# Kernel tuning notes

Measured on AMD Instinct MI355X. Metric: run time of the kernel, lower is better.

Reference implementation:

```python
import jax, jax.numpy as jnp
import numpy as np

D_MODEL = 768
D_INNER = 1536      # expand=2
D_STATE = 16
DT_RANK = 48        # ceil(768/16)
D_CONV = 4
DEPTH = 24
NUM_CLASSES = 527
GRID = (8, 64)      # (128/16, 1024/16)
SEQ = GRID[0] * GRID[1]
TOKPOS = SEQ // 2   # middle cls token position


def setup_inputs() -> dict:
    key = jax.random.key(0)
    ks = jax.random.split(key, 12)
    rn = lambda k, s, sc=0.02: jax.random.normal(k, s, jnp.float32) * sc
    A_init = jnp.log(jnp.arange(1, D_STATE + 1, dtype=jnp.float32))  # S4D-real init
    return {
        "x": jax.random.normal(ks[0], (1, 1, 128, 1024), jnp.float32),
        "patch_w": rn(ks[1], (D_MODEL, 1, 16, 16)),
        "patch_b": jnp.zeros((D_MODEL,), jnp.float32),
        "cls_token": rn(ks[2], (1, 1, D_MODEL)),
        "pos_embed": rn(ks[3], (1, SEQ + 1, D_MODEL)),
        "in_proj_w": rn(ks[4], (DEPTH, 2 * D_INNER, D_MODEL)),
        "conv_w": rn(ks[5], (DEPTH, 2, D_INNER, D_CONV), 0.1),
        "conv_b": jnp.zeros((DEPTH, 2, D_INNER), jnp.float32),
        "xproj_w": rn(ks[6], (DEPTH, 2, DT_RANK + 2 * D_STATE, D_INNER)),
        "dtproj_w": rn(ks[7], (DEPTH, 2, D_INNER, DT_RANK), 0.1),
        "dtproj_b": jnp.full((DEPTH, 2, D_INNER), float(np.log(np.expm1(0.01))), jnp.float32),
        "A_log": jnp.ones((DEPTH, 2, D_INNER, 1), jnp.float32) * A_init,
        "D_skip": jnp.ones((DEPTH, 2, D_INNER), jnp.float32),
        "out_proj_w": rn(ks[8], (DEPTH, D_MODEL, D_INNER)),
        "norm_w": jnp.ones((DEPTH, D_MODEL), jnp.float32),
        "norm_f_w": jnp.ones((D_MODEL,), jnp.float32),
        "head_w": rn(ks[9], (NUM_CLASSES, D_MODEL)),
        "head_b": jnp.zeros((NUM_CLASSES,), jnp.float32),
    }


def _rmsnorm(x, w, eps=1e-5):
    return x * jax.lax.rsqrt(jnp.mean(x * x, axis=-1, keepdims=True) + eps) * w


def _causal_conv_silu(x, w, b):
    # x [B,d,L], depthwise causal conv, kernel D_CONV, left-pad D_CONV-1
    L = x.shape[-1]
    xp = jnp.pad(x, ((0, 0), (0, 0), (D_CONV - 1, 0)))
    y = sum(w[:, k, None] * xp[:, :, k:k + L] for k in range(D_CONV)) + b[:, None]
    return jax.nn.silu(y)


def _selective_scan(dt, A, Bm, C, u):
    # dt,u: [B,d,L]; Bm,C: [B,N,L]; A: [d,N] (negative)
    def step(h, inp):
        dt_t, B_t, C_t, u_t = inp           # [B,d],[B,N],[B,N],[B,d]
        h = h * jnp.exp(dt_t[..., None] * A) + (dt_t * u_t)[..., None] * B_t[:, None, :]
        return h, jnp.einsum('bdn,bn->bd', h, C_t)
    h0 = jnp.zeros((dt.shape[0], A.shape[0], A.shape[1]), dt.dtype)
    mv = lambda a: jnp.moveaxis(a, -1, 0)
    _, ys = jax.lax.scan(step, h0, (mv(dt), mv(Bm), mv(C), mv(u)))
    return jnp.moveaxis(ys, 0, -1)          # [B,d,L]


def _mamba_dir(x, z, cw, cb, xw, dw, db, A_log, Dsk):
    xc = _causal_conv_silu(x, cw, cb)
    dbl = jnp.einsum('bdl,cd->bcl', xc, xw)                 # [B, R+2N, L]
    dt = jax.nn.softplus(jnp.einsum('brl,dr->bdl', dbl[:, :DT_RANK], dw) + db[:, None])
    Bm = dbl[:, DT_RANK:DT_RANK + D_STATE]
    C = dbl[:, DT_RANK + D_STATE:]
    y = _selective_scan(dt, -jnp.exp(A_log), Bm, C, xc) + Dsk[:, None] * xc
    return y * jax.nn.silu(z)


def _block(carry, p):
    hidden, residual = carry
    ipw, cw, cb, xw, dw, db, A_log, Dsk, opw, nw = p
    residual = residual + hidden                            # add -> norm -> mixer
    h = _rmsnorm(residual, nw)
    xz = jnp.einsum('bld,ed->ble', h, ipw)                  # [B,L,2*d_inner]
    x, z = jnp.split(jnp.moveaxis(xz, -1, 1), 2, axis=1)    # each [B,d_inner,L]
    yf = _mamba_dir(x, z, cw[0], cb[0], xw[0], dw[0], db[0], A_log[0], Dsk[0])
    yb = _mamba_dir(x[:, :, ::-1], z[:, :, ::-1], cw[1], cb[1], xw[1], dw[1],
                    db[1], A_log[1], Dsk[1])[:, :, ::-1]
    out = jnp.einsum('bdl,ed->ble', (yf + yb) * 0.5, opw)   # if_devide_out
    return (out, residual), None


def reference(x, patch_w, patch_b, cls_token, pos_embed, in_proj_w, conv_w, conv_b,
              xproj_w, dtproj_w, dtproj_b, A_log, D_skip, out_proj_w, norm_w,
              norm_f_w, head_w, head_b):
    h = jax.lax.conv_general_dilated(x, patch_w, (16, 16), 'VALID',
                                     dimension_numbers=('NCHW', 'OIHW', 'NCHW'))
    h = h + patch_b[None, :, None, None]
    B = h.shape[0]
    h = h.reshape(B, D_MODEL, SEQ).transpose(0, 2, 1)       # [B,512,768]
    cls = jnp.broadcast_to(cls_token, (B, 1, D_MODEL))
    h = jnp.concatenate([h[:, :TOKPOS], cls, h[:, TOKPOS:]], axis=1)  # [B,513,768]
    h = h + pos_embed
    carry = (h, jnp.zeros_like(h))
    (hidden, residual), _ = jax.lax.scan(
        _block, carry,
        (in_proj_w, conv_w, conv_b, xproj_w, dtproj_w, dtproj_b, A_log, D_skip,
         out_proj_w, norm_w))
    out = _rmsnorm(residual + hidden, norm_f_w)
    feat = out[:, TOKPOS]                                   # middle cls token
    return feat @ head_w.T + head_b
```

## Files before the change

kernel.cpp:

```cpp
#include <hip/hip_runtime.h>

#define L_SEQ 513
#define DM 768
#define DI 1536
#define DSTATE 16
#define DTRANK 48
#define NCLS 527
#define DEPTH 24
#define NC 32
#define CLEN 17
#define SKI 3
#define SKO 8

typedef unsigned short u16;
typedef __bf16 bf16x8 __attribute__((ext_vector_type(8)));
typedef float f32x4 __attribute__((ext_vector_type(4)));

#define MFMA_BF16(A, B, C) __builtin_amdgcn_mfma_f32_16x16x32_bf16(A, B, C, 0, 0, 0)

__device__ inline u16 f2bf(float x) {
  unsigned u = __float_as_uint(x);
  return (u16)((u + 0x7FFFu + ((u >> 16) & 1u)) >> 16);
}
__device__ inline float bf2f(u16 h) { return __uint_as_float((unsigned)h << 16); }
__device__ inline void split2(float v, u16& h, u16& l) {
  h = f2bf(v);
  l = f2bf(v - bf2f(h));
}
__device__ __forceinline__ int lofs(int row, int g) {
  int swz = (row & 3) ^ ((row >> 2) & 3);
  return row * 32 + ((g ^ swz) << 3);
}

__global__ void wconvert_kernel(const float* __restrict__ src,
                                u16* __restrict__ hi, u16* __restrict__ lo,
                                long n4) {
  long i = (long)blockIdx.x * 256 + threadIdx.x;
  long stride = (long)gridDim.x * 256;
  for (; i < n4; i += stride) {
    float4 v = ((const float4*)src)[i];
    ushort4 h, l;
    split2(v.x, h.x, l.x);
    split2(v.y, h.y, l.y);
    split2(v.z, h.z, l.z);
    split2(v.w, h.w, l.w);
    ((ushort4*)hi)[i] = h;
    ((ushort4*)lo)[i] = l;
  }
}

__global__ void patch_embed_kernel(const float* __restrict__ x,
                                   const float* __restrict__ pw,
                                   const float* __restrict__ pb,
                                   const float* __restrict__ cls,
                                   const float* __restrict__ pos,
                                   float* __restrict__ hidden,
                                   float* __restrict__ residual) {
  int c = blockIdx.x * 256 + threadIdx.x;
  int s = blockIdx.y;
  if (c >= DM) return;
  float val;
  if (s == 256) {
    val = cls[c];
  } else {
    int p = s - (s > 256 ? 1 : 0);
    int gy = p >> 6, gx = p & 63;
    const float* xp = x + gy * 16 * 1024 + gx * 16;
    const float* wp = pw + c * 256;
    float acc = pb[c];
#pragma unroll 4
    for (int ky = 0; ky < 16; ++ky)
#pragma unroll
      for (int kx = 0; kx < 16; ++kx)
        acc += xp[ky * 1024 + kx] * wp[ky * 16 + kx];
    val = acc;
  }
  long idx = (long)s * DM + c;
  hidden[idx] = val + pos[idx];
  residual[idx] = 0.f;
}

__global__ void rmsnorm_kernel(const float* __restrict__ hp, int nparts, long pstr,
                               float* __restrict__ residual,
                               u16* __restrict__ hnh, u16* __restrict__ hnl,
                               const float* __restrict__ w) {
  int t = blockIdx.x;
  float* rrow = residual + (long)t * DM;
  int tid = threadIdx.x;
  float vals[3];
  float ss = 0.f;
#pragma unroll
  for (int i = 0; i < 3; ++i) {
    int c = tid + i * 256;
    float v = rrow[c];
    for (int p = 0; p < nparts; ++p) v += hp[(long)p * pstr + (long)t * DM + c];
    vals[i] = v;
    rrow[c] = v;
    ss += v * v;
  }
#pragma unroll
  for (int o = 32; o; o >>= 1) ss += __shfl_down(ss, o, 64);
  __shared__ float sacc[4];
  if ((tid & 63) == 0) sacc[tid >> 6] = ss;
  __syncthreads();
  float tot = sacc[0] + sacc[1] + sacc[2] + sacc[3];
  float rs = rsqrtf(tot / (float)DM + 1e-5f);
#pragma unroll
  for (int i = 0; i < 3; ++i) {
    int c = tid + i * 256;
    float y = vals[i] * rs * w[c];
    u16 h, l;
    split2(y, h, l);
    hnh[(long)t * DM + c] = h;
    hnl[(long)t * DM + c] = l;
  }
}

template <int AMODE>
__global__ __launch_bounds__(256) void gemm128(
    const void* __restrict__ A0, const void* __restrict__ A1,
    const u16* __restrict__ Bh, const u16* __restrict__ Bl,
    float* __restrict__ C,
    int M, int N, int K, int lda, int ldb, int ldc,
    long sA, long sB, long sC, int NSK, int Kb, long sP) {
  int z = blockIdx.z;
  int batch = z / NSK, sk = z - batch * NSK;
  const u16* Ahb = nullptr;
  const u16* Alb = nullptr;
  const float* Af = nullptr;
  const float* Ag = nullptr;
  if (AMODE == 0) {
    Ahb = (const u16*)A0 + (long)batch * sA;
    Alb = (const u16*)A1 + (long)batch * sA;
  } else {
    Af = (const float*)A0 + (long)batch * sA;
    Ag = (const float*)A1 + (long)batch * sA;
  }
  const u16* Bhb = Bh + (long)batch * sB;
  const u16* Blb = Bl + (long)batch * sB;
  float* Cb = C + (long)batch * sC + (long)sk * sP;
  int ks0 = sk * Kb;
  int kend = min(ks0 + Kb, K);

  __shared__ u16 SA[2][2][128 * 32];
  __shared__ u16 SB[2][2][128 * 32];

  int tid = threadIdx.x;
  int m0 = blockIdx.y * 128, n0 = blockIdx.x * 128;

  int r0 = tid >> 2, g0 = tid & 3;
  int r1 = r0 + 64;
  int l0 = lofs(r0, g0), l1 = lofs(r1, g0);
  long aoff0 = (long)(m0 + r0) * lda, aoff1 = (long)(m0 + r1) * lda;
  long boff0 = (long)(n0 + r0) * ldb, boff1 = (long)(n0 + r1) * ldb;
  bool am0 = (m0 + r0) < M, am1 = (m0 + r1) < M;
  bool bm0 = (n0 + r0) < N, bm1 = (n0 + r1) < N;

  int lane = tid & 63, w = tid >> 6;
  int wr = w >> 1, wc = w & 1;
  int fr = lane & 15, kh = lane >> 4;
  int offA[4], offB[4];
#pragma unroll
  for (int i = 0; i < 4; ++i) {
    offA[i] = lofs(wr * 64 + i * 16 + fr, kh);
    offB[i] = lofs(wc * 64 + i * 16 + fr, kh);
  }

// ... 22 lines not shown
      ll = *(const uint4*)la;
    }
  };
  auto loadstep = [&](int kb) {
    int k_ = kb + g0 * 8;
    bool kk = (k_ + 8 <= kend);
    uint4 z4 = {0, 0, 0, 0};
    loadA(aoff0, kk && am0, k_, a0h, a0l);
    loadA(aoff1, kk && am1, k_, a1h, a1l);
    b0h = (kk && bm0) ? *(const uint4*)(Bhb + boff0 + k_) : z4;
    b1h = (kk && bm1) ? *(const uint4*)(Bhb + boff1 + k_) : z4;
    b0l = (kk && bm0) ? *(const uint4*)(Blb + boff0 + k_) : z4;
    b1l = (kk && bm1) ? *(const uint4*)(Blb + boff1 + k_) : z4;
  };
  auto writebuf = [&](int b) {
    *(uint4*)&SA[b][0][l0] = a0h;
    *(uint4*)&SA[b][0][l1] = a1h;
    *(uint4*)&SA[b][1][l0] = a0l;
    *(uint4*)&SA[b][1][l1] = a1l;
    *(uint4*)&SB[b][0][l0] = b0h;
    *(uint4*)&SB[b][0][l1] = b1h;
    *(uint4*)&SB[b][1][l0] = b0l;
    *(uint4*)&SB[b][1][l1] = b1l;
  };

  f32x4 acc[4][4] = {};
  int nst = (kend - ks0 + 31) >> 5;
  loadstep(ks0);
  writebuf(0);
  if (nst > 1) loadstep(ks0 + 32);
  __syncthreads();

  for (int s = 0; s < nst; ++s) {
    int b = s & 1;
    bf16x8 fah[4], fal[4], fbh[4], fbl[4];
#pragma unroll
    for (int i = 0; i < 4; ++i) {
      fah[i] = __builtin_bit_cast(bf16x8, *(const uint4*)&SA[b][0][offA[i]]);
      fal[i] = __builtin_bit_cast(bf16x8, *(const uint4*)&SA[b][1][offA[i]]);
      fbh[i] = __builtin_bit_cast(bf16x8, *(const uint4*)&SB[b][0][offB[i]]);
      fbl[i] = __builtin_bit_cast(bf16x8, *(const uint4*)&SB[b][1][offB[i]]);
    }
#pragma unroll
    for (int mi = 0; mi < 4; ++mi)
#pragma unroll
      for (int ni = 0; ni < 4; ++ni) {
        acc[mi][ni] = MFMA_BF16(fah[mi], fbh[ni], acc[mi][ni]);
        acc[mi][ni] = MFMA_BF16(fah[mi], fbl[ni], acc[mi][ni]);
        acc[mi][ni] = MFMA_BF16(fal[mi], fbh[ni], acc[mi][ni]);
      }
    if (s + 1 < nst) {
      writebuf(b ^ 1);
      if (s + 2 < nst) loadstep(ks0 + (s + 2) * 32);
    }
    __syncthreads();
  }

#pragma unroll
  for (int mi = 0; mi < 4; ++mi)
#pragma unroll
    for (int ni = 0; ni < 4; ++ni) {
      int n = n0 + wc * 64 + ni * 16 + fr;
      if (n >= N) continue;
#pragma unroll
      for (int r = 0; r < 4; ++r) {
        int m = m0 + wr * 64 + mi * 16 + kh * 4 + r;
        if (m >= M) continue;
        Cb[(long)m * ldc + n] = acc[mi][ni][r];
      }
    }
}

__global__ void conv_silu_kernel(const float* __restrict__ xz_p,
                                 const float* __restrict__ cw,
                                 const float* __restrict__ cb,
                                 float* __restrict__ xc,
                                 u16* __restrict__ xch, u16* __restrict__ xcl) {
  const long PZ = (long)L_SEQ * 2 * DI;
  int dir = blockIdx.y;
  int idx = blockIdx.x * 256 + threadIdx.x;
  if (idx >= L_SEQ * (DI / 4)) return;
  int d4 = idx % (DI / 4);
  int t = idx / (DI / 4);
  int d = d4 * 4;
  float wv[4][4];
#pragma unroll
  for (int j = 0; j < 4; ++j) {
    float4 wr = *(const float4*)(cw + ((long)dir * DI + d + j) * 4);
    wv[j][0] = wr.x; wv[j][1] = wr.y; wv[j][2] = wr.z; wv[j][3] = wr.w;
  }
  float4 bv = *(const float4*)(cb + (long)dir * DI + d);
  float a0 = bv.x, a1 = bv.y, a2 = bv.z, a3 = bv.w;
#pragma unroll
  for (int k = 0; k < 4; ++k) {
    int tau = t + k - 3;
    if (tau >= 0) {
      int tsrc = dir ? (L_SEQ - 1 - tau) : tau;
      long o = (long)tsrc * (2 * DI) + d;
      float4 x0 = *(const float4*)(xz_p + o);
      float4 x1 = *(const float4*)(xz_p + o + PZ);
      float4 x2 = *(const float4*)(xz_p + o + 2 * PZ);
      a0 += wv[0][k] * (x0.x + x1.x + x2.x);
      a1 += wv[1][k] * (x0.y + x1.y + x2.y);
      a2 += wv[2][k] * (x0.z + x1.z + x2.z);
      a3 += wv[3][k] * (x0.w + x1.w + x2.w);
    }
  }
  float4 sv;
  sv.x = a0 / (1.f + __expf(-a0));
  sv.y = a1 / (1.f + __expf(-a1));
  sv.z = a2 / (1.f + __expf(-a2));
  sv.w = a3 / (1.f + __expf(-a3));
  long o = ((long)dir * L_SEQ + t) * DI + d;
  *(float4*)(xc + o) = sv;
  ushort4 h, l;
  split2(sv.x, h.x, l.x);
  split2(sv.y, h.y, l.y);
  split2(sv.z, h.z, l.z);
  split2(sv.w, h.w, l.w);
  *(ushort4*)(xch + o) = h;
  *(ushort4*)(xcl + o) = l;
}

__global__ __launch_bounds__(256) void scan_all(
    const float* __restrict__ xc,
    const float* __restrict__ dbl,
    const float* __restrict__ xz_p,
    const float* __restrict__ dtw,
    const float* __restrict__ dtb,
    const float* __restrict__ A_log,
    const float* __restrict__ Dsk,
    float* __restrict__ y) {
  const long PZ = (long)L_SEQ * 2 * DI;
  int dir = blockIdx.y;
  int d0 = blockIdx.x * 8;
  int tid = threadIdx.x;
  __shared__ float Q[8][NC][DSTATE];
  __shared__ float Sv[8][NC];

  const float* xcp = xc + (long)dir * L_SEQ * DI;
  const float* dblp = dbl + (long)dir * L_SEQ * 80;

  int dl = tid & 7, c = tid >> 3;
  int d = d0 + dl;
  float negA[DSTATE];
#pragma unroll
  for (int n = 0; n < DSTATE; ++n)
    negA[n] = -__expf(A_log[((long)dir * DI + d) * DSTATE + n]);
  float4 dwr[12];
  {
    const float4* dwp = (const float4*)(dtw + ((long)dir * DI + d) * DTRANK);
#pragma unroll
    for (int q = 0; q < 12; ++q) dwr[q] = dwp[q];
  }
  float db_ = dtb[(long)dir * DI + d];

  int t0 = c * CLEN, t1 = min(t0 + CLEN, L_SEQ);

  {
    float h[DSTATE];
#pragma unroll
    for (int n = 0; n < DSTATE; ++n) h[n] = 0.f;
    float S = 0.f;
    for (int t = t0; t < t1; ++t) {
      const float4* R = (const float4*)(dblp + (long)t * 80);
      float dot = db_;
#pragma unroll
      for (int q = 0; q < 12; ++q) {
        float4 r4 = R[q];
        dot += r4.x * dwr[q].x + r4.y * dwr[q].y + r4.z * dwr[q].z + r4.w * dwr[q].w;
      }
      float dt = (dot > 20.f) ? dot : log1pf(__expf(dot));
      float u = xcp[(long)t * DI + d];
      float du = dt * u;
      S += dt;
      float4 b0 = R[12], b1 = R[13], b2 = R[14], b3 = R[15];
      float Bv[DSTATE] = {b0.x, b0.y, b0.z, b0.w, b1.x, b1.y, b1.z, b1.w,
                          b2.x, b2.y, b2.z, b2.w, b3.x, b3.y, b3.z, b3.w};
#pragma unroll
      for (int n = 0; n < DSTATE; ++n)
        h[n] = h[n] * __expf(dt * negA[n]) + du * Bv[n];
    }
    Sv[dl][c] = S;
#pragma unroll
    for (int n = 0; n < DSTATE; ++n) Q[dl][c][n] = h[n];
  }
  __syncthreads();
  if (tid < 128) {
    int fdl = tid >> 4, n = tid & 15;
    int fd = d0 + fdl;
    float nA = -__expf(A_log[((long)dir * DI + fd) * DSTATE + n]);
    float h = 0.f;
    for (int cc = 0; cc < NC; ++cc) {
      float S = Sv[fdl][cc];
      float q = Q[fdl][cc][n];
      Q[fdl][cc][n] = h;
      h = h * __expf(nA * S) + q;
    }
  }
  __syncthreads();
  {
    float h[DSTATE];
#pragma unroll
    for (int n = 0; n < DSTATE; ++n) h[n] = Q[dl][c][n];
    float dskip = Dsk[(long)dir * DI + d];
    for (int t = t0; t < t1; ++t) {
      const float4* R = (const float4*)(dblp + (long)t * 80);
      float dot = db_;
#pragma unroll
      for (int q = 0; q < 12; ++q) {
        float4 r4 = R[q];
        dot += r4.x * dwr[q].x + r4.y * dwr[q].y + r4.z * dwr[q].z + r4.w * dwr[q].w;
      }
      float dt = (dot > 20.f) ? dot : log1pf(__expf(dot));
      float u = xcp[(long)t * DI + d];
      float du = dt * u;
      float4 b0 = R[12], b1 = R[13], b2 = R[14], b3 = R[15];
      float4 c0 = R[16], c1 = R[17], c2 = R[18], c3 = R[19];
      float Bv[DSTATE] = {b0.x, b0.y, b0.z, b0.w, b1.x, b1.y, b1.z, b1.w,
                          b2.x, b2.y, b2.z, b2.w, b3.x, b3.y, b3.z, b3.w};
      float Cv[DSTATE] = {c0.x, c0.y, c0.z, c0.w, c1.x, c1.y, c1.z, c1.w,
                          c2.x, c2.y, c2.z, c2.w, c3.x, c3.y, c3.z, c3.w};
      float acc = 0.f;
#pragma unroll
      for (int n = 0; n < DSTATE; ++n) {
        h[n] = h[n] * __expf(dt * negA[n]) + du * Bv[n];
        acc += h[n] * Cv[n];
      }
      int tsrc = dir ? (L_SEQ - 1 - t) : t;
      long zo = (long)tsrc * (2 * DI) + DI + d;
      float zv = xz_p[zo] + xz_p[zo + PZ] + xz_p[zo + 2 * PZ];
      float sz = zv / (1.f + __expf(-zv));
      y[((long)dir * L_SEQ + tsrc) * DI + d] = (acc + dskip * u) * sz;
    }
  }
}

__global__ void head_kernel(const float* __restrict__ residual,
                            const float* __restrict__ hp, long pstr,
                            const float* __restrict__ nfw,
                            const float* __restrict__ hw,
                            const float* __restrict__ hb,
                            float* __restrict__ out) {
  int j = blockIdx.x;
  int tid = threadIdx.x;
  const float* r = residual + (long)256 * DM;
  float ss = 0.f, dp = 0.f;
#pragma unroll
  for (int i = 0; i < 3; ++i) {
    int c = tid + i * 256;
    float v = r[c];
    for (int p = 0; p < SKO; ++p) v += hp[(long)p * pstr + (long)256 * DM + c];
    ss += v * v;
    dp += v * nfw[c] * hw[(long)j * DM + c];
  }
#pragma unroll
  for (int o = 32; o; o >>= 1) {
    ss += __shfl_down(ss, o, 64);
    dp += __shfl_down(dp, o, 64);
  }
  __shared__ float s1[4], s2[4];
  if ((tid & 63) == 0) {
    s1[tid >> 6] = ss;
    s2[tid >> 6] = dp;
  }
  __syncthreads();
  if (tid == 0) {
    float tot = s1[0] + s1[1] + s1[2] + s1[3];
    float d = s2[0] + s2[1] + s2[2] + s2[3];
    out[j] = d * rsqrtf(tot / (float)DM + 1e-5f) + hb[j];
  }
}

extern "C" void kernel_launch(void* const* d_in, const int* in_sizes, int n_in,
                              void* d_out, int out_size, void* d_ws, size_t ws_size,
                              hipStream_t stream) {
  const float* x        = (const float*)d_in[0];
  const float* patch_w  = (const float*)d_in[1];
  const float* patch_b  = (const float*)d_in[2];
  const float* cls_tok  = (const float*)d_in[3];
  const float* pos_emb  = (const float*)d_in[4];
  const float* in_proj  = (const float*)d_in[5];
  const float* conv_w   = (const float*)d_in[6];
  const float* conv_b   = (const float*)d_in[7];
  const float* xproj_w  = (const float*)d_in[8];
  const float* dtproj_w = (const float*)d_in[9];
  const float* dtproj_b = (const float*)d_in[10];
  const float* A_log    = (const float*)d_in[11];
  const float* D_skip   = (const float*)d_in[12];
  const float* out_proj = (const float*)d_in[13];
  const float* norm_w   = (const float*)d_in[14];
  const float* norm_f_w = (const float*)d_in[15];
  const float* head_w   = (const float*)d_in[16];
  const float* head_b   = (const float*)d_in[17];
  float* out = (float*)d_out;

  const long PHN = (long)L_SEQ * DM;
  const long PZ  = (long)L_SEQ * 2 * DI;

  float* ws = (float*)d_ws;
  float* residual = ws; ws += PHN;
  float* xz_p     = ws; ws += SKI * PZ;
  float* xc       = ws; ws += (long)2 * L_SEQ * DI;
  float* dbl      = ws; ws += (long)2 * L_SEQ * 80;
  float* yb       = ws; ws += (long)2 * L_SEQ * DI;
  float* hid_p    = ws; ws += (long)SKO * PHN;

  u16* wsu = (u16*)ws;
  const long N_HN = PHN;
  const long N_XC = (long)2 * L_SEQ * DI;
  const long N_WI = (long)DEPTH * 2 * DI * DM;
  const long N_WX = (long)DEPTH * 2 * 80 * DI;
  const long N_WO = (long)DEPTH * DM * DI;
  u16* hn_h = wsu; wsu += N_HN;
  u16* hn_l = wsu; wsu += N_HN;
  u16* xc_h = wsu; wsu += N_XC;
  u16* xc_l = wsu; wsu += N_XC;
  u16* wi_h = wsu; wsu += N_WI;
  u16* wi_l = wsu; wsu += N_WI;
  u16* wx_h = wsu; wsu += N_WX;
  u16* wx_l = wsu; wsu += N_WX;
  u16* wo_h = wsu; wsu += N_WO;
  u16* wo_l = wsu; wsu += N_WO;

  wconvert_kernel<<<2048, 256, 0, stream>>>(in_proj,  wi_h, wi_l, N_WI / 4);
  wconvert_kernel<<<512,  256, 0, stream>>>(xproj_w,  wx_h, wx_l, N_WX / 4);
  wconvert_kernel<<<2048, 256, 0, stream>>>(out_proj, wo_h, wo_l, N_WO / 4);

  patch_embed_kernel<<<dim3(3, L_SEQ), 256, 0, stream>>>(
      x, patch_w, patch_b, cls_tok, pos_emb, hid_p, residual);

  for (int l = 0; l < DEPTH; ++l) {
    const u16* wih = wi_h + (long)l * 2 * DI * DM;
    const u16* wil = wi_l + (long)l * 2 * DI * DM;
    const u16* wxh = wx_h + (long)l * 2 * 80 * DI;
    const u16* wxl = wx_l + (long)l * 2 * 80 * DI;
    const u16* woh = wo_h + (long)l * DM * DI;
    const u16* wol = wo_l + (long)l * DM * DI;
    const float* cw  = conv_w   + (long)l * 2 * DI * 4;
    const float* cb  = conv_b   + (long)l * 2 * DI;
    const float* dw  = dtproj_w + (long)l * 2 * DI * DTRANK;
    const float* db  = dtproj_b + (long)l * 2 * DI;
    const float* Al  = A_log    + (long)l * 2 * DI * DSTATE;
    const float* Dk  = D_skip   + (long)l * 2 * DI;
    const float* nw  = norm_w   + (long)l * DM;

    rmsnorm_kernel<<<L_SEQ, 256, 0, stream>>>(
        hid_p, (l == 0) ? 1 : SKO, PHN, residual, hn_h, hn_l, nw);

    gemm128<0><<<dim3(24, 5, SKI), 256, 0, stream>>>(
        hn_h, hn_l, wih, wil, xz_p, L_SEQ, 2 * DI, DM, DM, DM, 2 * DI,
        0, 0, 0, SKI, DM / SKI, PZ);

    conv_silu_kernel<<<dim3(770, 2), 256, 0, stream>>>(xz_p, cw, cb, xc, xc_h, xc_l);

    gemm128<0><<<dim3(1, 5, 2), 256, 0, stream>>>(
        xc_h, xc_l, wxh, wxl, dbl, L_SEQ, 80, DI, DI, DI, 80,
        (long)L_SEQ * DI, (long)80 * DI, (long)L_SEQ * 80, 1, DI, 0);

    scan_all<<<dim3(DI / 8, 2), 256, 0, stream>>>(
        xc, dbl, xz_p, dw, db, Al, Dk, yb);

    gemm128<1><<<dim3(6, 5, SKO), 256, 0, stream>>>(
        yb, yb + (long)L_SEQ * DI, woh, wol, hid_p, L_SEQ, DM, DI, DI, DI, DM,
        0, 0, 0, SKO, DI / SKO, PHN);
  }

  head_kernel<<<NCLS, 256, 0, stream>>>(residual, hid_p, PHN,
                                        norm_f_w, head_w, head_b, out);
}
```

Before: 4.750 ms.

## Fuse all layers into a persistent megakernel with software grid barriers

Replaces the per-layer sequence of six kernel launches with one persistent kernel of 256 blocks that loops over all 24 layers. Stages are separated by an atomic-flag grid barrier, which removes roughly 144 launch gaps. The dt projection becomes an MFMA GEMM with a fused softplus epilogue, z-gating SiLU is precomputed in the conv stage, and the in_proj split-K drops from 3 to 2. The cost is low parallelism in small stages such as the 10-tile x_proj GEMM and the scan, which leave most blocks idle. The software barrier also depends on all 256 blocks being co-resident.

```diff
diff --git a/kernel.cpp b/kernel.cpp
--- a/kernel.cpp
+++ b/kernel.cpp
@@ -9,10 +9,12 @@
 #define DEPTH 24
 #define NC 32
 #define CLEN 17
-#define SKI 3
+#define SKI 2
 #define SKO 8
+#define NBLK 256
 
 typedef unsigned short u16;
+typedef unsigned int u32;
 typedef __bf16 bf16x8 __attribute__((ext_vector_type(8)));
 typedef float f32x4 __attribute__((ext_vector_type(4)));
 
@@ -31,126 +33,51 @@
   int swz = (row & 3) ^ ((row >> 2) & 3);
   return row * 32 + ((g ^ swz) << 3);
 }
-
-__global__ void wconvert_kernel(const float* __restrict__ src,
-                                u16* __restrict__ hi, u16* __restrict__ lo,
-                                long n4) {
-  long i = (long)blockIdx.x * 256 + threadIdx.x;
-  long stride = (long)gridDim.x * 256;
-  for (; i < n4; i += stride) {
-    float4 v = ((const float4*)src)[i];
-    ushort4 h, l;
-    split2(v.x, h.x, l.x);
-    split2(v.y, h.y, l.y);
-    split2(v.z, h.z, l.z);
-    split2(v.w, h.w, l.w);
-    ((ushort4*)hi)[i] = h;
-    ((ushort4*)lo)[i] = l;
+__device__ inline float siluf(float v) { return v / (1.f + __expf(-v)); }
+
+__device__ __forceinline__ void grid_sync(u32* flags, u32* epoch, u32 e) {
+  __syncthreads();
+  if (blockIdx.x == 0) {
+    if (threadIdx.x == 0)
+      __hip_atomic_store(&flags[0], e, __ATOMIC_RELEASE, __HIP_MEMORY_SCOPE_AGENT);
+    int b = threadIdx.x;
+    while (__hip_atomic_load(&flags[b * 16], __ATOMIC_ACQUIRE, __HIP_MEMORY_SCOPE_AGENT) < e)
+      __builtin_amdgcn_s_sleep(1);
+    __syncthreads();
+    if (threadIdx.x == 0)
+      __hip_atomic_store(epoch, e, __ATOMIC_RELEASE, __HIP_MEMORY_SCOPE_AGENT);
+  } else {
+    if (threadIdx.x == 0) {
+      __hip_atomic_store(&flags[blockIdx.x * 16], e, __ATOMIC_RELEASE, __HIP_MEMORY_SCOPE_AGENT);
+      while (__hip_atomic_load(epoch, __ATOMIC_ACQUIRE, __HIP_MEMORY_SCOPE_AGENT) < e)
+        __builtin_amdgcn_s_sleep(1);
+    }
   }
-}
-
-__global__ void patch_embed_kernel(const float* __restrict__ x,
-                                   const float* __restrict__ pw,
-                                   const float* __restrict__ pb,
-                                   const float* __restrict__ cls,
-                                   const float* __restrict__ pos,
-                                   float* __restrict__ hidden,
-                                   float* __restrict__ residual) {
-  int c = blockIdx.x * 256 + threadIdx.x;
-  int s = blockIdx.y;
-  if (c >= DM) return;
-  float val;
-  if (s == 256) {
-    val = cls[c];
-  } else {
-    int p = s - (s > 256 ? 1 : 0);
-    int gy = p >> 6, gx = p & 63;
-    const float* xp = x + gy * 16 * 1024 + gx * 16;
-    const float* wp = pw + c * 256;
-    float acc = pb[c];
-#pragma unroll 4
-    for (int ky = 0; ky < 16; ++ky)
-#pragma unroll
-      for (int kx = 0; kx < 16; ++kx)
-        acc += xp[ky * 1024 + kx] * wp[ky * 16 + kx];
-    val = acc;
-  }
-  long idx = (long)s * DM + c;
-  hidden[idx] = val + pos[idx];
-  residual[idx] = 0.f;
-}
-
-__global__ void rmsnorm_kernel(const float* __restrict__ hp, int nparts, long pstr,
-                               float* __restrict__ residual,
-                               u16* __restrict__ hnh, u16* __restrict__ hnl,
-                               const float* __restrict__ w) {
-  int t = blockIdx.x;
-  float* rrow = residual + (long)t * DM;
+  __syncthreads();
+}
+
+template <int AMODE>
+__device__ void gemm_tile(const void* A0, const void* A1,
+                          const u16* __restrict__ Bh, const u16* __restrict__ Bl,
+                          float* __restrict__ Cb, int M, int N, int K,
+                          int lda, int ldb, int ldc,
+                          int m0, int n0, int ks0, int kend,
+                          const float* biasp, int act,
+                          u16* d48h, u16* d48l, int ncap, int ldhl,
+                          u16* LDSU) {
+  u16* SA = LDSU;
+  u16* SB = LDSU + 16384;
+
   int tid = threadIdx.x;
-  float vals[3];
-  float ss = 0.f;
-#pragma unroll
-  for (int i = 0; i < 3; ++i) {
-    int c = tid + i * 256;
-    float v = rrow[c];
-    for (int p = 0; p < nparts; ++p) v += hp[(long)p * pstr + (long)t * DM + c];
-    vals[i] = v;
-    rrow[c] = v;
-    ss += v * v;
-  }
-#pragma unroll
-  for (int o = 32; o; o >>= 1) ss += __shfl_down(ss, o, 64);
-  __shared__ float sacc[4];
-  if ((tid & 63) == 0) sacc[tid >> 6] = ss;
-  __syncthreads();
-  float tot = sacc[0] + sacc[1] + sacc[2] + sacc[3];
-  float rs = rsqrtf(tot / (float)DM + 1e-5f);
-#pragma unroll
-  for (int i = 0; i < 3; ++i) {
-    int c = tid + i * 256;
-    float y = vals[i] * rs * w[c];
-    u16 h, l;
-    split2(y, h, l);
-    hnh[(long)t * DM + c] = h;
-    hnl[(long)t * DM + c] = l;
-  }
-}
-
-template <int AMODE>
-__global__ __launch_bounds__(256) void gemm128(
-    const void* __restrict__ A0, const void* __restrict__ A1,
-    const u16* __restrict__ Bh, const u16* __restrict__ Bl,
-    float* __restrict__ C,
-    int M, int N, int K, int lda, int ldb, int ldc,
-    long sA, long sB, long sC, int NSK, int Kb, long sP) {
-  int z = blockIdx.z;
-  int batch = z / NSK, sk = z - batch * NSK;
-  const u16* Ahb = nullptr;
-  const u16* Alb = nullptr;
-  const float* Af = nullptr;
-  const float* Ag = nullptr;
-  if (AMODE == 0) {
-    Ahb = (const u16*)A0 + (long)batch * sA;
-    Alb = (const u16*)A1 + (long)batch * sA;
-  } else {
-    Af = (const float*)A0 + (long)batch * sA;
-    Ag = (const float*)A1 + (long)batch * sA;
-  }
-  const u16* Bhb = Bh + (long)batch * sB;
-  const u16* Blb = Bl + (long)batch * sB;
-  float* Cb = C + (long)batch * sC + (long)sk * sP;
-  int ks0 = sk * Kb;
-  int kend = min(ks0 + Kb, K);
-
-  __shared__ u16 SA[2][2][128 * 32];
-  __shared__ u16 SB[2][2][128 * 32];
-
-  int tid = threadIdx.x;
-  int m0 = blockIdx.y * 128, n0 = blockIdx.x * 128;
-
   int r0 = tid >> 2, g0 = tid & 3;
   int r1 = r0 + 64;
   int l0 = lofs(r0, g0), l1 = lofs(r1, g0);
+  const u16* Ahb = (const u16*)A0;
+  const u16* Alb = (const u16*)A1;
+  const float* Af = (const float*)A0;
+  const float* Ag = (const float*)A1;
+  const u16* Bhb = Bh;
+  const u16* Blb = Bl;
   long aoff0 = (long)(m0 + r0) * lda, aoff1 = (long)(m0 + r1) * lda;
   long boff0 = (long)(n0 + r0) * ldb, boff1 = (long)(n0 + r1) * ldb;
   bool am0 = (m0 + r0) < M, am1 = (m0 + r1) < M;
@@ -203,14 +130,14 @@
     b1l = (kk && bm1) ? *(const uint4*)(Blb + boff1 + k_) : z4;
   };
   auto writebuf = [&](int b) {
-    *(uint4*)&SA[b][0][l0] = a0h;
-    *(uint4*)&SA[b][0][l1] = a1h;
-    *(uint4*)&SA[b][1][l0] = a0l;
-    *(uint4*)&SA[b][1][l1] = a1l;
-    *(uint4*)&SB[b][0][l0] = b0h;
-    *(uint4*)&SB[b][0][l1] = b1h;
-    *(uint4*)&SB[b][1][l0] = b0l;
-    *(uint4*)&SB[b][1][l1] = b1l;
+    *(uint4*)&SA[((b << 1) | 0) * 4096 + l0] = a0h;
+    *(uint4*)&SA[((b << 1) | 0) * 4096 + l1] = a1h;
+    *(uint4*)&SA[((b << 1) | 1) * 4096 + l0] = a0l;
+    *(uint4*)&SA[((b << 1) | 1) * 4096 + l1] = a1l;
+    *(uint4*)&SB[((b << 1) | 0) * 4096 + l0] = b0h;
+    *(uint4*)&SB[((b << 1) | 0) * 4096 + l1] = b1h;
+    *(uint4*)&SB[((b << 1) | 1) * 4096 + l0] = b0l;
+    *(uint4*)&SB[((b << 1) | 1) * 4096 + l1] = b1l;
   };
 
   f32x4 acc[4][4] = {};
@@ -225,10 +152,10 @@
     bf16x8 fah[4], fal[4], fbh[4], fbl[4];
 #pragma unroll
     for (int i = 0; i < 4; ++i) {
-      fah[i] = __builtin_bit_cast(bf16x8, *(const uint4*)&SA[b][0][offA[i]]);
-      fal[i] = __builtin_bit_cast(bf16x8, *(const uint4*)&SA[b][1][offA[i]]);
-      fbh[i] = __builtin_bit_cast(bf16x8, *(const uint4*)&SB[b][0][offB[i]]);
-      fbl[i] = __builtin_bit_cast(bf16x8, *(const uint4*)&SB[b][1][offB[i]]);
+      fah[i] = __builtin_bit_cast(bf16x8, *(const uint4*)&SA[((b << 1) | 0) * 4096 + offA[i]]);
+      fal[i] = __builtin_bit_cast(bf16x8, *(const uint4*)&SA[((b << 1) | 1) * 4096 + offA[i]]);
+      fbh[i] = __builtin_bit_cast(bf16x8, *(const uint4*)&SB[((b << 1) | 0) * 4096 + offB[i]]);
+      fbl[i] = __builtin_bit_cast(bf16x8, *(const uint4*)&SB[((b << 1) | 1) * 4096 + offB[i]]);
     }
 #pragma unroll
     for (int mi = 0; mi < 4; ++mi)
@@ -251,213 +178,360 @@
     for (int ni = 0; ni < 4; ++ni) {
       int n = n0 + wc * 64 + ni * 16 + fr;
       if (n >= N) continue;
+      float bv = biasp ? biasp[n] : 0.f;
 #pragma unroll
       for (int r = 0; r < 4; ++r) {
         int m = m0 + wr * 64 + mi * 16 + kh * 4 + r;
         if (m >= M) continue;
-        Cb[(long)m * ldc + n] = acc[mi][ni][r];
-      }
-    }
-}
-
-__global__ void conv_silu_kernel(const float* __restrict__ xz_p,
-                                 const float* __restrict__ cw,
-                                 const float* __restrict__ cb,
-                                 float* __restrict__ xc,
-                                 u16* __restrict__ xch, u16* __restrict__ xcl) {
+        float v = acc[mi][ni][r] + bv;
+        if (act == 1) v = (v > 20.f) ? v : log1pf(__expf(v));
+        Cb[(long)m * ldc + n] = v;
+        if (d48h && n < ncap) {
+          u16 hh, ll;
+          split2(v, hh, ll);
+          d48h[(long)m * ldhl + n] = hh;
+          d48l[(long)m * ldhl + n] = ll;
+        }
+      }
+    }
+}
+
+__global__ void wconvert_kernel(const float* __restrict__ src,
+                                u16* __restrict__ hi, u16* __restrict__ lo,
+                                long n4) {
+  long i = (long)blockIdx.x * 256 + threadIdx.x;
+  long stride = (long)gridDim.x * 256;
+  for (; i < n4; i += stride) {
+    float4 v = ((const float4*)src)[i];
+    ushort4 h, l;
+    split2(v.x, h.x, l.x);
+    split2(v.y, h.y, l.y);
+    split2(v.z, h.z, l.z);
+    split2(v.w, h.w, l.w);
+    ((ushort4*)hi)[i] = h;
+    ((ushort4*)lo)[i] = l;
+  }
+}
+
+__global__ void patch_embed_kernel(const float* __restrict__ x,
+                                   const float* __restrict__ pw,
+                                   const float* __restrict__ pb,
+                                   const float* __restrict__ cls,
+                                   const float* __restrict__ pos,
+                                   float* __restrict__ hidden,
+                                   float* __restrict__ residual) {
+  int c = blockIdx.x * 256 + threadIdx.x;
+  int s = blockIdx.y;
+  if (c >= DM) return;
+  float val;
+  if (s == 256) {
+    val = cls[c];
+  } else {
+    int p = s - (s > 256 ? 1 : 0);
+    int gy = p >> 6, gx = p & 63;
+    const float* xp = x + gy * 16 * 1024 + gx * 16;
+    const float* wp = pw + c * 256;
+    float acc = pb[c];
+#pragma unroll 4
+    for (int ky = 0; ky < 16; ++ky)
+#pragma unroll
+      for (int kx = 0; kx < 16; ++kx)
+        acc += xp[ky * 1024 + kx] * wp[ky * 16 + kx];
+    val = acc;
+  }
+  long idx = (long)s * DM + c;
+  hidden[idx] = val + pos[idx];
+  residual[idx] = 0.f;
+}
+
+__global__ __launch_bounds__(256, 2) void mega(
+    const float* __restrict__ conv_w, const float* __restrict__ conv_b,
+    const float* __restrict__ dtproj_b, const float* __restrict__ A_log,
+    const float* __restrict__ D_skip, const float* __restrict__ norm_w,
+    const float* __restrict__ norm_f_w, const float* __restrict__ head_w,
+    const float* __restrict__ head_b,
+    float* residual, float* xz_p, float* xc, float* zs, float* dbl,
+    float* dtb, float* yb, float* hid_p,
+    u16* hn_h, u16* hn_l, u16* xc_h, u16* xc_l, u16* d48_h, u16* d48_l,
+    const u16* wi_h, const u16* wi_l, const u16* wx_h, const u16* wx_l,
+    const u16* wd_h, const u16* wd_l, const u16* wo_h, const u16* wo_l,
+    u32* flags, u32* epoch, float* out) {
+  __shared__ __align__(16) u16 LDSU[32768];
+  const int bid = blockIdx.x;
+  const int tid = threadIdx.x;
+  const long PHN = (long)L_SEQ * DM;
   const long PZ = (long)L_SEQ * 2 * DI;
-  int dir = blockIdx.y;
-  int idx = blockIdx.x * 256 + threadIdx.x;
-  if (idx >= L_SEQ * (DI / 4)) return;
-  int d4 = idx % (DI / 4);
-  int t = idx / (DI / 4);
-  int d = d4 * 4;
-  float wv[4][4];
-#pragma unroll
-  for (int j = 0; j < 4; ++j) {
-    float4 wr = *(const float4*)(cw + ((long)dir * DI + d + j) * 4);
-    wv[j][0] = wr.x; wv[j][1] = wr.y; wv[j][2] = wr.z; wv[j][3] = wr.w;
+  const long LDIlen = (long)L_SEQ * DI;
+  u32 e = 0;
+
+  for (int l = 0; l < DEPTH; ++l) {
+    const u16* wih = wi_h + (long)l * 2 * DI * DM;
+    const u16* wil = wi_l + (long)l * 2 * DI * DM;
+    const u16* wxh = wx_h + (long)l * 2 * 80 * DI;
+    const u16* wxl = wx_l + (long)l * 2 * 80 * DI;
+    const u16* wdh = wd_h + (long)l * 2 * DI * DTRANK;
+    const u16* wdl = wd_l + (long)l * 2 * DI * DTRANK;
+    const u16* woh = wo_h + (long)l * DM * DI;
+    const u16* wol = wo_l + (long)l * DM * DI;
+    const float* cw = conv_w + (long)l * 2 * DI * 4;
+    const float* cb = conv_b + (long)l * 2 * DI;
+    const float* db = dtproj_b + (long)l * 2 * DI;
+    const float* Al = A_log + (long)l * 2 * DI * DSTATE;
+    const float* Dk = D_skip + (long)l * 2 * DI;
+    const float* nw = norm_w + (long)l * DM;
+    int nparts = (l == 0) ? 1 : SKO;
+
+    for (int t = bid; t < L_SEQ; t += NBLK) {
+      float* rrow = residual + (long)t * DM;
+      float vals[3];
+      float ss = 0.f;
+#pragma unroll
+      for (int i = 0; i < 3; ++i) {
+        int c = tid + i * 256;
+        float v = rrow[c];
+        for (int p = 0; p < nparts; ++p) v += hid_p[(long)p * PHN + (long)t * DM + c];
+        vals[i] = v;
+        rrow[c] = v;
+        ss += v * v;
+      }
+#pragma unroll
+      for (int o = 32; o; o >>= 1) ss += __shfl_down(ss, o, 64);
+      float* sacc = (float*)LDSU;
+      if ((tid & 63) == 0) sacc[tid >> 6] = ss;
+      __syncthreads();
+      float tot = sacc[0] + sacc[1] + sacc[2] + sacc[3];
+      float rs = rsqrtf(tot / (float)DM + 1e-5f);
+      __syncthreads();
+#pragma unroll
+      for (int i = 0; i < 3; ++i) {
+        int c = tid + i * 256;
+        float y = vals[i] * rs * nw[c];
+        u16 h, lo;
+        split2(y, h, lo);
+        hn_h[(long)t * DM + c] = h;
+        hn_l[(long)t * DM + c] = lo;
+      }
+    }
+    e++; grid_sync(flags, epoch, e);
+
+    for (int vt = bid; vt < 24 * 5 * SKI; vt += NBLK) {
+      int sk = vt & (SKI - 1), rest = vt >> 1;
+      int my = rest / 24, nx = rest % 24;
+      gemm_tile<0>(hn_h, hn_l, wih, wil, xz_p + (long)sk * PZ,
+                   L_SEQ, 2 * DI, DM, DM, DM, 2 * DI,
+                   my * 128, nx * 128, sk * 384, min(DM, sk * 384 + 384),
+                   nullptr, 0, nullptr, nullptr, 0, 0, LDSU);
+    }
+    e++; grid_sync(flags, epoch, e);
+
+    for (int v = bid; v < 2310; v += NBLK) {
+      if (v < 1540) {
+        int dir = v / 770, vv = v - dir * 770;
+        int idx = vv * 256 + tid;
+        if (idx < L_SEQ * (DI / 4)) {
+          int d4 = idx % (DI / 4);
+          int t = idx / (DI / 4);
+          int d = d4 * 4;
+          float wv[4][4];
+#pragma unroll
+          for (int j = 0; j < 4; ++j) {
+            float4 wr4 = *(const float4*)(cw + ((long)dir * DI + d + j) * 4);
+            wv[j][0] = wr4.x; wv[j][1] = wr4.y; wv[j][2] = wr4.z; wv[j][3] = wr4.w;
+          }
+          float4 bv = *(const float4*)(cb + (long)dir * DI + d);
+          float a0 = bv.x, a1 = bv.y, a2 = bv.z, a3 = bv.w;
+#pragma unroll
+          for (int k = 0; k < 4; ++k) {
+            int tau = t + k - 3;
+            if (tau >= 0) {
+              int tsrc = dir ? (L_SEQ - 1 - tau) : tau;
+              long o = (long)tsrc * (2 * DI) + d;
+              float4 x0 = *(const float4*)(xz_p + o);
+              float4 x1 = *(const float4*)(xz_p + o + PZ);
+              a0 += wv[0][k] * (x0.x + x1.x);
+              a1 += wv[1][k] * (x0.y + x1.y);
+              a2 += wv[2][k] * (x0.z + x1.z);
+              a3 += wv[3][k] * (x0.w + x1.w);
+            }
+          }
+          float4 sv;
+          sv.x = siluf(a0); sv.y = siluf(a1); sv.z = siluf(a2); sv.w = siluf(a3);
+          long o = ((long)dir * L_SEQ + t) * DI + d;
+          *(float4*)(xc + o) = sv;
+          ushort4 h, lo;
+          split2(sv.x, h.x, lo.x);
+          split2(sv.y, h.y, lo.y);
+          split2(sv.z, h.z, lo.z);
+          split2(sv.w, h.w, lo.w);
+          *(ushort4*)(xc_h + o) = h;
+          *(ushort4*)(xc_l + o) = lo;
+        }
+      } else {
+        int vv = v - 1540;
+        int idx = vv * 256 + tid;
+        if (idx < L_SEQ * (DI / 4)) {
+          int d4 = idx % (DI / 4);
+          int t = idx / (DI / 4);
+          long zo = (long)t * (2 * DI) + DI + d4 * 4;
+          float4 z0 = *(const float4*)(xz_p + zo);
+          float4 z1 = *(const float4*)(xz_p + zo + PZ);
+          float4 sv;
+          sv.x = siluf(z0.x + z1.x);
+          sv.y = siluf(z0.y + z1.y);
+          sv.z = siluf(z0.z + z1.z);
+          sv.w = siluf(z0.w + z1.w);
+          *(float4*)(zs + (long)t * DI + d4 * 4) = sv;
+        }
+      }
+    }
+    e++; grid_sync(flags, epoch, e);
+
+    if (bid < 10) {
+      int dir = bid / 5, my = bid % 5;
+      gemm_tile<0>(xc_h + dir * LDIlen, xc_l + dir * LDIlen,
+                   wxh + (long)dir * 80 * DI, wxl + (long)dir * 80 * DI,
+                   dbl + (long)dir * L_SEQ * 80,
+                   L_SEQ, 80, DI, DI, DI, 80,
+                   my * 128, 0, 0, DI,
+                   nullptr, 0,
+                   d48_h + (long)dir * L_SEQ * DTRANK,
+                   d48_l + (long)dir * L_SEQ * DTRANK, DTRANK, DTRANK, LDSU);
+    }
+    e++; grid_sync(flags, epoch, e);
+
+    for (int vt = bid; vt < 120; vt += NBLK) {
+      int dir = vt / 60, r = vt - dir * 60;
+      int my = r / 12, nx = r % 12;
+      gemm_tile<0>(d48_h + (long)dir * L_SEQ * DTRANK, d48_l + (long)dir * L_SEQ * DTRANK,
+                   wdh + (long)dir * DI * DTRANK, wdl + (long)dir * DI * DTRANK,
+                   dtb + dir * LDIlen,
+                   L_SEQ, DI, DTRANK, DTRANK, DTRANK, DI,
+                   my * 128, nx * 128, 0, DTRANK,
+                   db + dir * DI, 1, nullptr, nullptr, 0, 0, LDSU);
+    }
+    e++; grid_sync(flags, epoch, e);
+
+    for (int vb = bid; vb < 384; vb += NBLK) {
+      int dir = vb / 192, d0 = (vb - dir * 192) * 8;
+      float* Q = (float*)LDSU;
+      float* Sv = (float*)LDSU + 4096;
+      const float* dtp = dtb + dir * LDIlen;
+      const float* xcp = xc + dir * LDIlen;
+      const float* dblp = dbl + (long)dir * L_SEQ * 80;
+      int dl = tid & 7, c = tid >> 3;
+      int d = d0 + dl;
+      float negA[DSTATE];
+#pragma unroll
+      for (int n = 0; n < DSTATE; ++n)
+        negA[n] = -__expf(Al[((long)dir * DI + d) * DSTATE + n]);
+      int t0 = c * CLEN, t1 = min(t0 + CLEN, L_SEQ);
+      {
+        float h[DSTATE];
+#pragma unroll
+        for (int n = 0; n < DSTATE; ++n) h[n] = 0.f;
+        float S = 0.f;
+        for (int t = t0; t < t1; ++t) {
+          float dt = dtp[(long)t * DI + d];
+          float u = xcp[(long)t * DI + d];
+          float du = dt * u;
+          S += dt;
+          const float4* B4 = (const float4*)(dblp + (long)t * 80 + DTRANK);
+          float4 b0 = B4[0], b1 = B4[1], b2 = B4[2], b3 = B4[3];
+          float Bv[DSTATE] = {b0.x, b0.y, b0.z, b0.w, b1.x, b1.y, b1.z, b1.w,
+                              b2.x, b2.y, b2.z, b2.w, b3.x, b3.y, b3.z, b3.w};
+#pragma unroll
+          for (int n = 0; n < DSTATE; ++n)
+            h[n] = h[n] * __expf(dt * negA[n]) + du * Bv[n];
+        }
+        Sv[dl * NC + c] = S;
+#pragma unroll
+        for (int n = 0; n < DSTATE; ++n) Q[(dl * NC + c) * DSTATE + n] = h[n];
+      }
+      __syncthreads();
+      if (tid < 128) {
+        int fdl = tid >> 4, n = tid & 15;
+        int fd = d0 + fdl;
+        float nA = -__expf(Al[((long)dir * DI + fd) * DSTATE + n]);
+        float h = 0.f;
+        for (int cc = 0; cc < NC; ++cc) {
+          float S = Sv[fdl * NC + cc];
+          float q = Q[(fdl * NC + cc) * DSTATE + n];
+          Q[(fdl * NC + cc) * DSTATE + n] = h;
+          h = h * __expf(nA * S) + q;
+        }
+      }
+      __syncthreads();
+      {
+        float h[DSTATE];
+#pragma unroll
+        for (int n = 0; n < DSTATE; ++n) h[n] = Q[(dl * NC + c) * DSTATE + n];
+        float dskip = Dk[(long)dir * DI + d];
+        for (int t = t0; t < t1; ++t) {
+          float dt = dtp[(long)t * DI + d];
+          float u = xcp[(long)t * DI + d];
+          float du = dt * u;
+          const float4* B4 = (const float4*)(dblp + (long)t * 80 + DTRANK);
+          float4 b0 = B4[0], b1 = B4[1], b2 = B4[2], b3 = B4[3];
+          float4 c0 = B4[4], c1 = B4[5], c2 = B4[6], c3 = B4[7];
+          float Bv[DSTATE] = {b0.x, b0.y, b0.z, b0.w, b1.x, b1.y, b1.z, b1.w,
+                              b2.x, b2.y, b2.z, b2.w, b3.x, b3.y, b3.z, b3.w};
+          float Cv[DSTATE] = {c0.x, c0.y, c0.z, c0.w, c1.x, c1.y, c1.z, c1.w,
+                              c2.x, c2.y, c2.z, c2.w, c3.x, c3.y, c3.z, c3.w};
+          float acc = 0.f;
+#pragma unroll
+          for (int n = 0; n < DSTATE; ++n) {
+            h[n] = h[n] * __expf(dt * negA[n]) + du * Bv[n];
+            acc += h[n] * Cv[n];
+          }
+          int tsrc = dir ? (L_SEQ - 1 - t) : t;
+          float sz = zs[(long)tsrc * DI + d];
+          yb[((long)dir * L_SEQ + tsrc) * DI + d] = (acc + dskip * u) * sz;
+        }
+      }
+      __syncthreads();
+    }
+    e++; grid_sync(flags, epoch, e);
+
+    for (int vt = bid; vt < 240; vt += NBLK) {
+      int sk = vt & 7, rest = vt >> 3;
+      int my = rest / 6, nx = rest % 6;
+      gemm_tile<1>(yb, yb + LDIlen, woh, wol, hid_p + (long)sk * PHN,
+                   L_SEQ, DM, DI, DI, DI, DM,
+                   my * 128, nx * 128, sk * 192, sk * 192 + 192,
+                   nullptr, 0, nullptr, nullptr, 0, 0, LDSU);
+    }
+    e++; grid_sync(flags, epoch, e);
   }
-  float4 bv = *(const float4*)(cb + (long)dir * DI + d);
-  float a0 = bv.x, a1 = bv.y, a2 = bv.z, a3 = bv.w;
-#pragma unroll
-  for (int k = 0; k < 4; ++k) {
-    int tau = t + k - 3;
-    if (tau >= 0) {
-      int tsrc = dir ? (L_SEQ - 1 - tau) : tau;
-      long o = (long)tsrc * (2 * DI) + d;
-      float4 x0 = *(const float4*)(xz_p + o);
-      float4 x1 = *(const float4*)(xz_p + o + PZ);
-      float4 x2 = *(const float4*)(xz_p + o + 2 * PZ);
-      a0 += wv[0][k] * (x0.x + x1.x + x2.x);
-      a1 += wv[1][k] * (x0.y + x1.y + x2.y);
-      a2 += wv[2][k] * (x0.z + x1.z + x2.z);
-      a3 += wv[3][k] * (x0.w + x1.w + x2.w);
-    }
-  }
-  float4 sv;
-  sv.x = a0 / (1.f + __expf(-a0));
-  sv.y = a1 / (1.f + __expf(-a1));
-  sv.z = a2 / (1.f + __expf(-a2));
-  sv.w = a3 / (1.f + __expf(-a3));
-  long o = ((long)dir * L_SEQ + t) * DI + d;
-  *(float4*)(xc + o) = sv;
-  ushort4 h, l;
-  split2(sv.x, h.x, l.x);
-  split2(sv.y, h.y, l.y);
-  split2(sv.z, h.z, l.z);
-  split2(sv.w, h.w, l.w);
-  *(ushort4*)(xch + o) = h;
-  *(ushort4*)(xcl + o) = l;
-}
-
-__global__ __launch_bounds__(256) void scan_all(
-    const float* __restrict__ xc,
-    const float* __restrict__ dbl,
-    const float* __restrict__ xz_p,
-    const float* __restrict__ dtw,
-    const float* __restrict__ dtb,
-    const float* __restrict__ A_log,
-    const float* __restrict__ Dsk,
-    float* __restrict__ y) {
-  const long PZ = (long)L_SEQ * 2 * DI;
-  int dir = blockIdx.y;
-  int d0 = blockIdx.x * 8;
-  int tid = threadIdx.x;
-  __shared__ float Q[8][NC][DSTATE];
-  __shared__ float Sv[8][NC];
-
-  const float* xcp = xc + (long)dir * L_SEQ * DI;
-  const float* dblp = dbl + (long)dir * L_SEQ * 80;
-
-  int dl = tid & 7, c = tid >> 3;
-  int d = d0 + dl;
-  float negA[DSTATE];
-#pragma unroll
-  for (int n = 0; n < DSTATE; ++n)
-    negA[n] = -__expf(A_log[((long)dir * DI + d) * DSTATE + n]);
-  float4 dwr[12];
-  {
-    const float4* dwp = (const float4*)(dtw + ((long)dir * DI + d) * DTRANK);
-#pragma unroll
-    for (int q = 0; q < 12; ++q) dwr[q] = dwp[q];
-  }
-  float db_ = dtb[(long)dir * DI + d];
-
-  int t0 = c * CLEN, t1 = min(t0 + CLEN, L_SEQ);
-
-  {
-    float h[DSTATE];
-#pragma unroll
-    for (int n = 0; n < DSTATE; ++n) h[n] = 0.f;
-    float S = 0.f;
-    for (int t = t0; t < t1; ++t) {
-      const float4* R = (const float4*)(dblp + (long)t * 80);
-      float dot = db_;
-#pragma unroll
-      for (int q = 0; q < 12; ++q) {
-        float4 r4 = R[q];
-        dot += r4.x * dwr[q].x + r4.y * dwr[q].y + r4.z * dwr[q].z + r4.w * dwr[q].w;
-      }
-      float dt = (dot > 20.f) ? dot : log1pf(__expf(dot));
-      float u = xcp[(long)t * DI + d];
-      float du = dt * u;
-      S += dt;
-      float4 b0 = R[12], b1 = R[13], b2 = R[14], b3 = R[15];
-      float Bv[DSTATE] = {b0.x, b0.y, b0.z, b0.w, b1.x, b1.y, b1.z, b1.w,
-                          b2.x, b2.y, b2.z, b2.w, b3.x, b3.y, b3.z, b3.w};
-#pragma unroll
-      for (int n = 0; n < DSTATE; ++n)
-        h[n] = h[n] * __expf(dt * negA[n]) + du * Bv[n];
-    }
-    Sv[dl][c] = S;
-#pragma unroll
-    for (int n = 0; n < DSTATE; ++n) Q[dl][c][n] = h[n];
-  }
-  __syncthreads();
-  if (tid < 128) {
-    int fdl = tid >> 4, n = tid & 15;
-    int fd = d0 + fdl;
-    float nA = -__expf(A_log[((long)dir * DI + fd) * DSTATE + n]);
-    float h = 0.f;
-    for (int cc = 0; cc < NC; ++cc) {
-      float S = Sv[fdl][cc];
-      float q = Q[fdl][cc][n];
-      Q[fdl][cc][n] = h;
-      h = h * __expf(nA * S) + q;
-    }
-  }
-  __syncthreads();
-  {
-    float h[DSTATE];
-#pragma unroll
-    for (int n = 0; n < DSTATE; ++n) h[n] = Q[dl][c][n];
-    float dskip = Dsk[(long)dir * DI + d];
-    for (int t = t0; t < t1; ++t) {
-      const float4* R = (const float4*)(dblp + (long)t * 80);
-      float dot = db_;
-#pragma unroll
-      for (int q = 0; q < 12; ++q) {
-        float4 r4 = R[q];
-        dot += r4.x * dwr[q].x + r4.y * dwr[q].y + r4.z * dwr[q].z + r4.w * dwr[q].w;
-      }
-      float dt = (dot > 20.f) ? dot : log1pf(__expf(dot));
-      float u = xcp[(long)t * DI + d];
-      float du = dt * u;
-      float4 b0 = R[12], b1 = R[13], b2 = R[14], b3 = R[15];
-      float4 c0 = R[16], c1 = R[17], c2 = R[18], c3 = R[19];
-      float Bv[DSTATE] = {b0.x, b0.y, b0.z, b0.w, b1.x, b1.y, b1.z, b1.w,
-                          b2.x, b2.y, b2.z, b2.w, b3.x, b3.y, b3.z, b3.w};
-      float Cv[DSTATE] = {c0.x, c0.y, c0.z, c0.w, c1.x, c1.y, c1.z, c1.w,
-                          c2.x, c2.y, c2.z, c2.w, c3.x, c3.y, c3.z, c3.w};
-      float acc = 0.f;
-#pragma unroll
-      for (int n = 0; n < DSTATE; ++n) {
-        h[n] = h[n] * __expf(dt * negA[n]) + du * Bv[n];
-        acc += h[n] * Cv[n];
-      }
-      int tsrc = dir ? (L_SEQ - 1 - t) : t;
-      long zo = (long)tsrc * (2 * DI) + DI + d;
-      float zv = xz_p[zo] + xz_p[zo + PZ] + xz_p[zo + 2 * PZ];
-      float sz = zv / (1.f + __expf(-zv));
-      y[((long)dir * L_SEQ + tsrc) * DI + d] = (acc + dskip * u) * sz;
-    }
-  }
-}
-
-__global__ void head_kernel(const float* __restrict__ residual,
-                            const float* __restrict__ hp, long pstr,
-                            const float* __restrict__ nfw,
-                            const float* __restrict__ hw,
-                            const float* __restrict__ hb,
-                            float* __restrict__ out) {
-  int j = blockIdx.x;
-  int tid = threadIdx.x;
-  const float* r = residual + (long)256 * DM;
-  float ss = 0.f, dp = 0.f;
-#pragma unroll
-  for (int i = 0; i < 3; ++i) {
-    int c = tid + i * 256;
-    float v = r[c];
-    for (int p = 0; p < SKO; ++p) v += hp[(long)p * pstr + (long)256 * DM + c];
-    ss += v * v;
-    dp += v * nfw[c] * hw[(long)j * DM + c];
-  }
-#pragma unroll
-  for (int o = 32; o; o >>= 1) {
-    ss += __shfl_down(ss, o, 64);
-    dp += __shfl_down(dp, o, 64);
-  }
-  __shared__ float s1[4], s2[4];
-  if ((tid & 63) == 0) {
-    s1[tid >> 6] = ss;
-    s2[tid >> 6] = dp;
-  }
-  __syncthreads();
-  if (tid == 0) {
-    float tot = s1[0] + s1[1] + s1[2] + s1[3];
-    float d = s2[0] + s2[1] + s2[2] + s2[3];
-    out[j] = d * rsqrtf(tot / (float)DM + 1e-5f) + hb[j];
+
+  for (int j = bid; j < NCLS; j += NBLK) {
+    const float* r = residual + (long)256 * DM;
+    float ss = 0.f, dp = 0.f;
+#pragma unroll
+    for (int i = 0; i < 3; ++i) {
+      int c = tid + i * 256;
+      float v = r[c];
+      for (int p = 0; p < SKO; ++p) v += hid_p[(long)p * PHN + (long)256 * DM + c];
+      ss += v * v;
+      dp += v * norm_f_w[c] * head_w[(long)j * DM + c];
+    }
+#pragma unroll
+    for (int o = 32; o; o >>= 1) {
+      ss += __shfl_down(ss, o, 64);
+      dp += __shfl_down(dp, o, 64);
+    }
+    float* s1 = (float*)LDSU;
+    float* s2 = (float*)LDSU + 8;
+    if ((tid & 63) == 0) {
+      s1[tid >> 6] = ss;
+      s2[tid >> 6] = dp;
+    }
+    __syncthreads();
+    if (tid == 0) {
+      float tot = s1[0] + s1[1] + s1[2] + s1[3];
+      float dd = s2[0] + s2[1] + s2[2] + s2[3];
+      out[j] = dd * rsqrtf(tot / (float)DM + 1e-5f) + head_b[j];
+    }
+    __syncthreads();
   }
 }
 
@@ -487,74 +561,56 @@
   const long PHN = (long)L_SEQ * DM;
   const long PZ  = (long)L_SEQ * 2 * DI;
 
-  float* ws = (float*)d_ws;
-  float* residual = ws; ws += PHN;
-  float* xz_p     = ws; ws += SKI * PZ;
-  float* xc       = ws; ws += (long)2 * L_SEQ * DI;
-  float* dbl      = ws; ws += (long)2 * L_SEQ * 80;
-  float* yb       = ws; ws += (long)2 * L_SEQ * DI;
-  float* hid_p    = ws; ws += (long)SKO * PHN;
-
-  u16* wsu = (u16*)ws;
+  char* base = (char*)d_ws;
+  u32* flags = (u32*)base;
+  u32* epoch = (u32*)(base + NBLK * 64);
+  float* fb = (float*)(base + 32768);
+  float* residual = fb; fb += PHN;
+  float* xz_p     = fb; fb += SKI * PZ;
+  float* xc       = fb; fb += (long)2 * L_SEQ * DI;
+  float* zs       = fb; fb += (long)L_SEQ * DI;
+  float* dbl      = fb; fb += (long)2 * L_SEQ * 80;
+  float* dtb      = fb; fb += (long)2 * L_SEQ * DI;
+  float* yb       = fb; fb += (long)2 * L_SEQ * DI;
+  float* hid_p    = fb; fb += (long)SKO * PHN;
+
+  u16* wsu = (u16*)fb;
   const long N_HN = PHN;
   const long N_XC = (long)2 * L_SEQ * DI;
+  const long N_D48 = (long)2 * L_SEQ * DTRANK;
   const long N_WI = (long)DEPTH * 2 * DI * DM;
   const long N_WX = (long)DEPTH * 2 * 80 * DI;
+  const long N_WD = (long)DEPTH * 2 * DI * DTRANK;
   const long N_WO = (long)DEPTH * DM * DI;
   u16* hn_h = wsu; wsu += N_HN;
   u16* hn_l = wsu; wsu += N_HN;
   u16* xc_h = wsu; wsu += N_XC;
   u16* xc_l = wsu; wsu += N_XC;
+  u16* d48_h = wsu; wsu += N_D48;
+  u16* d48_l = wsu; wsu += N_D48;
   u16* wi_h = wsu; wsu += N_WI;
   u16* wi_l = wsu; wsu += N_WI;
   u16* wx_h = wsu; wsu += N_WX;
   u16* wx_l = wsu; wsu += N_WX;
+  u16* wd_h = wsu; wsu += N_WD;
+  u16* wd_l = wsu; wsu += N_WD;
   u16* wo_h = wsu; wsu += N_WO;
   u16* wo_l = wsu; wsu += N_WO;
 
+  (void)hipMemsetAsync(d_ws, 0, 32768, stream);
+
   wconvert_kernel<<<2048, 256, 0, stream>>>(in_proj,  wi_h, wi_l, N_WI / 4);
   wconvert_kernel<<<512,  256, 0, stream>>>(xproj_w,  wx_h, wx_l, N_WX / 4);
+  wconvert_kernel<<<512,  256, 0, stream>>>(dtproj_w, wd_h, wd_l, N_WD / 4);
   wconvert_kernel<<<2048, 256, 0, stream>>>(out_proj, wo_h, wo_l, N_WO / 4);
 
   patch_embed_kernel<<<dim3(3, L_SEQ), 256, 0, stream>>>(
       x, patch_w, patch_b, cls_tok, pos_emb, hid_p, residual);
 
-  for (int l = 0; l < DEPTH; ++l) {
-    const u16* wih = wi_h + (long)l * 2 * DI * DM;
-    const u16* wil = wi_l + (long)l * 2 * DI * DM;
-    const u16* wxh = wx_h + (long)l * 2 * 80 * DI;
-    const u16* wxl = wx_l + (long)l * 2 * 80 * DI;
-    const u16* woh = wo_h + (long)l * DM * DI;
-    const u16* wol = wo_l + (long)l * DM * DI;
-    const float* cw  = conv_w   + (long)l * 2 * DI * 4;
-    const float* cb  = conv_b   + (long)l * 2 * DI;
-    const float* dw  = dtproj_w + (long)l * 2 * DI * DTRANK;
-    const float* db  = dtproj_b + (long)l * 2 * DI;
-    const float* Al  = A_log    + (long)l * 2 * DI * DSTATE;
-    const float* Dk  = D_skip   + (long)l * 2 * DI;
-    const float* nw  = norm_w   + (long)l * DM;
-
-    rmsnorm_kernel<<<L_SEQ, 256, 0, stream>>>(
-        hid_p, (l == 0) ? 1 : SKO, PHN, residual, hn_h, hn_l, nw);
-
-    gemm128<0><<<dim3(24, 5, SKI), 256, 0, stream>>>(
-        hn_h, hn_l, wih, wil, xz_p, L_SEQ, 2 * DI, DM, DM, DM, 2 * DI,
-        0, 0, 0, SKI, DM / SKI, PZ);
-
-    conv_silu_kernel<<<dim3(770, 2), 256, 0, stream>>>(xz_p, cw, cb, xc, xc_h, xc_l);
-
-    gemm128<0><<<dim3(1, 5, 2), 256, 0, stream>>>(
-        xc_h, xc_l, wxh, wxl, dbl, L_SEQ, 80, DI, DI, DI, 80,
-        (long)L_SEQ * DI, (long)80 * DI, (long)L_SEQ * 80, 1, DI, 0);
-
-    scan_all<<<dim3(DI / 8, 2), 256, 0, stream>>>(
-        xc, dbl, xz_p, dw, db, Al, Dk, yb);
-
-    gemm128<1><<<dim3(6, 5, SKO), 256, 0, stream>>>(
-        yb, yb + (long)L_SEQ * DI, woh, wol, hid_p, L_SEQ, DM, DI, DI, DI, DM,
-        0, 0, 0, SKO, DI / SKO, PHN);
-  }
-
-  head_kernel<<<NCLS, 256, 0, stream>>>(residual, hid_p, PHN,
-                                        norm_f_w, head_w, head_b, out);
-}
+  mega<<<NBLK, 256, 0, stream>>>(
+      conv_w, conv_b, dtproj_b, A_log, D_skip, norm_w, norm_f_w, head_w, head_b,
+      residual, xz_p, xc, zs, dbl, dtb, yb, hid_p,
+      hn_h, hn_l, xc_h, xc_l, d48_h, d48_l,
+      wi_h, wi_l, wx_h, wx_l, wd_h, wd_l, wo_h, wo_l,
+      flags, epoch, out);
+}
```

Result: slower. 18.19 ms (+282.9%).
